# Kernel tuning notes

Hardware: AMD Instinct MI355X
Metric: run time of the kernel (lower is better)

The kernel has to match this reference:

```python
import jax, jax.numpy as jnp
import numpy as np

L, B, N_IN, N_OUT, BIDIR, K = 2048, 16, 256, 256, 2, 6


def setup_inputs() -> dict:
    key = jax.random.key(0)
    k1, k2 = jax.random.split(key, 2)
    x = jax.random.normal(k1, (L, B, N_IN), jnp.float32)
    val = (6.0 / (N_IN + N_OUT)) ** 0.5
    weight_in = jax.random.uniform(k2, (N_IN, BIDIR * N_OUT * K), jnp.float32, -val, val)
    bias_in = jnp.zeros((K * BIDIR * N_OUT,), jnp.float32)
    c1_init = jnp.zeros((B, BIDIR * N_OUT), jnp.float32)
    c2_init = jnp.zeros((B, BIDIR * N_OUT), jnp.float32)
    d_init = jnp.zeros((B, BIDIR * N_OUT), jnp.float32)
    return {"x": x, "weight_in": weight_in, "bias_in": bias_in,
            "c1_init": c1_init, "c2_init": c2_init, "d_init": d_init}


def _flip_dir1(a):
    # reverse time for the backward direction (dir index 1)
    return a.at[:, :, 1].set(jnp.flip(a[:, :, 1], axis=0))


def _sopa_forward(x, weight_in, bias_in, c1_init, c2_init, d_init):
    length, batch = x.shape[0], x.shape[1]
    # u_: [L, B, bidir, n_out, k]
    u = (x.reshape(-1, N_IN) @ weight_in).reshape(length, batch, BIDIR, N_OUT, K)
    bias = bias_in.reshape(K, BIDIR, N_OUT)  # [k, bidir, n_out]
    x1, x2, x3 = u[..., 0], u[..., 1], u[..., 2]
    f1 = jax.nn.sigmoid(u[..., 3] + bias[3])
    f2 = jax.nn.sigmoid(u[..., 4] + bias[4])
    # selfloop gate sigmoid(u[...,5]+bias[5]) is computed in the original but
    # unused by the recurrence, so it is omitted here (no effect on outputs).

    # flip time for direction 1 so one scan handles both directions
    x1f, x2f, x3f, f1f, f2f = (_flip_dir1(a) for a in (x1, x2, x3, f1, f2))

    c1_0 = c1_init.reshape(batch, BIDIR, N_OUT)
    c2_0 = c2_init.reshape(batch, BIDIR, N_OUT)
    d_0 = d_init.reshape(batch, BIDIR, N_OUT)

    def step(carry, inp):
        c1, c2, d = carry
        x1t, x2t, x3t, f1t, f2t = inp
        c1n = (c1 - x1t) * f1t + x1t
        tmp = x3t * d
        c2n = (c2 - tmp) * f2t + tmp
        return (c1n, c2n, x2t), (c1n, c2n)

    (c1_f, c2_f, d_f), (c1s, c2s) = jax.lax.scan(
        step, (c1_0, c2_0, d_0), (x1f, x2f, x3f, f1f, f2f))

    c1s = _flip_dir1(c1s)
    c2s = _flip_dir1(c2s)
    return (c1s, c2s,
            c1_f.reshape(batch, -1), c2_f.reshape(batch, -1), d_f.reshape(batch, -1))


def reference(x, weight_in, bias_in, c1_init, c2_init, d_init):
    return _sopa_forward(x, weight_in, bias_in, c1_init, c2_init, d_init)
```

## Files before the change

### kernel.cpp

```cpp
#include <hip/hip_runtime.h>
#include <cstdint>
#include <cstddef>

typedef unsigned short u16;
typedef unsigned int u32;
typedef __bf16 bf16x8 __attribute__((ext_vector_type(8)));
typedef float f32x4 __attribute__((ext_vector_type(4)));

#define SL 2048
#define NCH 8192
#define SEGS 64

#define OFF_C2S 16777216
#define OFF_C1F 33554432
#define OFF_C2F 33562624
#define OFF_DF  33570816

__device__ __forceinline__ u16 f2bf(float f) {
  union { float f; u32 i; } v; v.f = f;
  u32 x = v.i;
  return (u16)((x + 0x7fffu + ((x >> 16) & 1u)) >> 16);
}
__device__ __forceinline__ u32 cvtpk(float lo, float hi) {
  u32 r;
  asm("v_cvt_pk_bf16_f32 %0, %1, %2" : "=v"(r) : "v"(lo), "v"(hi));
  return r;
}
__device__ __forceinline__ float sigmoidf(float v) {
  return 1.f / (1.f + __expf(-v));
}

__global__ __launch_bounds__(256) void xconv_kernel(
    const float* __restrict__ x, u16* __restrict__ xb) {
  int t8 = blockIdx.x * 256 + threadIdx.x;
  int b  = t8 & 15;
  int kb = (t8 >> 4) & 31;
  int ot = t8 >> 9;
  const float* src = x + (((size_t)(ot * 16 + b)) << 8) + kb * 8;
  f32x4 a = *(const f32x4*)src;
  f32x4 c = *(const f32x4*)(src + 4);
  union { bf16x8 v; u32 u[4]; } h;
  h.u[0] = cvtpk(a[0], a[1]);
  h.u[1] = cvtpk(a[2], a[3]);
  h.u[2] = cvtpk(c[0], c[1]);
  h.u[3] = cvtpk(c[2], c[3]);
  *(bf16x8*)(xb + ((size_t)ot << 12) + kb * 128 + b * 8) = h.v;
}

__global__ __launch_bounds__(256) void repack_kernel(
    const float* __restrict__ W, u16* __restrict__ Wt) {
  int idx = blockIdx.x * 256 + threadIdx.x;
  int col = idx % 3072;
  int kk  = idx / 3072;
  float w = W[idx];
  int d    = (col >= 1536) ? 1 : 0;
  int col2 = col - d * 1536;
  int n = col2 / 6;
  int p = col2 - n * 6;
  if (p >= 5) return;
  int ch2 = d * 256 + n;
  int cg = ch2 >> 4, l15 = ch2 & 15;
  int kk8 = kk & 7, q = kk >> 3;
  int l4 = q & 3, h = (q >> 2) & 1, kt = q >> 3;
  size_t dst = ((size_t)(p * 256 + cg * 8 + kt * 2 + h)) * 512 +
               (l4 * 16 + l15) * 8 + kk8;
  Wt[dst] = f2bf(w);
}

__global__ __launch_bounds__(256, 2) void fusedA_kernel(
    const u16* __restrict__ xb, const u16* __restrict__ Wt,
    const float* __restrict__ bias,
    float* __restrict__ A1, float* __restrict__ B1,
    float* __restrict__ A2, float* __restrict__ B2k,
    float* __restrict__ G2, float* __restrict__ X2B) {
  const int tid = threadIdx.x;
  const int lane = tid & 63;
  const int wc = tid >> 6;
  const int l15 = lane & 15, l4 = lane >> 4;
  const int bid = blockIdx.x;
  const int xcd = bid & 7;
  const int j = bid >> 3;
  const int s = xcd * 8 + (j & 7);
  const int bc = j >> 3;
  const int dir = bc >> 2;
  const int ch2 = bc * 64 + wc * 16 + l15;
  const int fb0 = (bc * 4 + wc) * 8;

  const float bv3 = bias[1536 + ch2];
  const float bv4 = bias[2048 + ch2];

  float a1[4], b1[4], a2[4], b2[4], g2[4], x2p[4];
#pragma unroll
  for (int r = 0; r < 4; ++r) {
    a1[r] = 1.f; b1[r] = 0.f; a2[r] = 1.f; b2[r] = 0.f;
    g2[r] = 0.f; x2p[r] = 0.f;
  }

  for (int rt = 0; rt < 8; ++rt) {
    const u16* ab0; const u16* ab1; const u16* ab2; const u16* ab3;
    {
      int tf = s * 32 + rt * 4;
      int o0 = dir ? (SL - 1 - tf) : tf;
      int o1 = dir ? (o0 - 1) : (o0 + 1);
      int o2 = dir ? (o0 - 2) : (o0 + 2);
      int o3 = dir ? (o0 - 3) : (o0 + 3);
      size_t lo = (size_t)(l4 * 128 + l15 * 8);
      ab0 = xb + ((size_t)o0 << 12) + lo;
      ab1 = xb + ((size_t)o1 << 12) + lo;
      ab2 = xb + ((size_t)o2 << 12) + lo;
      ab3 = xb + ((size_t)o3 << 12) + lo;
    }

    f32x4 acc[5][4];
#pragma unroll
    for (int p = 0; p < 5; ++p)
#pragma unroll
      for (int i = 0; i < 4; ++i) acc[p][i] = (f32x4){0.f, 0.f, 0.f, 0.f};

#pragma unroll
    for (int kt = 0; kt < 4; ++kt) {
#pragma unroll
      for (int h = 0; h < 2; ++h) {
        const int kb4 = (kt * 8 + h * 4) * 128;
        bf16x8 af[4];
        af[0] = *(const bf16x8*)(ab0 + kb4);
        af[1] = *(const bf16x8*)(ab1 + kb4);
        af[2] = *(const bf16x8*)(ab2 + kb4);
        af[3] = *(const bf16x8*)(ab3 + kb4);
        const int fb = fb0 + kt * 2 + h;
#pragma unroll
        for (int p = 0; p < 5; ++p) {
          bf16x8 bfr = *(const bf16x8*)(
              Wt + (size_t)(p * 256 + fb) * 512 + lane * 8);
#pragma unroll
          for (int i = 0; i < 4; ++i)
            acc[p][i] = __builtin_amdgcn_mfma_f32_16x16x32_bf16(
                af[i], bfr, acc[p][i], 0, 0, 0);
        }
      }
    }

    const bool first = (rt == 0);
#pragma unroll
    for (int i = 0; i < 4; ++i) {
#pragma unroll
      for (int r = 0; r < 4; ++r) {
        float x1 = acc[0][i][r], x2v = acc[1][i][r], x3 = acc[2][i][r];
        float f1 = sigmoidf(acc[3][i][r] + bv3);
        float f2 = sigmoidf(acc[4][i][r] + bv4);
        a1[r] *= f1;
        b1[r] = f1 * b1[r] + (1.f - f1) * x1;
        float tmp = x3 * x2p[r];
        a2[r] *= f2;
        b2[r] = f2 * b2[r] + (1.f - f2) * tmp;
        g2[r] = (first && i == 0) ? (1.f - f2) * x3 : g2[r] * f2;
        x2p[r] = x2v;
      }
    }
  }

  const size_t oo = (size_t)s * NCH + (size_t)ch2 * 16 + l4 * 4;
  *(f32x4*)(A1  + oo) = (f32x4){a1[0], a1[1], a1[2], a1[3]};
  *(f32x4*)(B1  + oo) = (f32x4){b1[0], b1[1], b1[2], b1[3]};
  *(f32x4*)(A2  + oo) = (f32x4){a2[0], a2[1], a2[2], a2[3]};
  *(f32x4*)(B2k + oo) = (f32x4){b2[0], b2[1], b2[2], b2[3]};
  *(f32x4*)(G2  + oo) = (f32x4){g2[0], g2[1], g2[2], g2[3]};
  *(f32x4*)(X2B + oo) = (f32x4){x2p[0], x2p[1], x2p[2], x2p[3]};
}

__global__ __launch_bounds__(256) void scanB_kernel(
    const float* __restrict__ A1, const float* __restrict__ B1,
    const float* __restrict__ A2, const float* __restrict__ B2k,
    const float* __restrict__ G2, const float* __restrict__ X2B,
    const float* __restrict__ c1_init, const float* __restrict__ c2_init,
    const float* __restrict__ d_init,
    float* __restrict__ C1c, float* __restrict__ C2c,
    float* __restrict__ out) {
  int t = blockIdx.x * 256 + threadIdx.x;
  int ch2 = t >> 4, b = t & 15;
  int ch = b * 512 + ch2;
  float c1 = c1_init[ch], c2 = c2_init[ch], d0 = d_init[ch];
#pragma unroll 8
  for (int s = 0; s < SEGS; ++s) {
    int o = s * NCH + t;
    C1c[o] = c1; C2c[o] = c2;
    c1 = A1[o] * c1 + B1[o];
    c2 = A2[o] * c2 + (B2k[o] + G2[o] * d0);
    d0 = X2B[o];
  }
  out[OFF_C1F + ch] = c1;
  out[OFF_C2F + ch] = c2;
  out[OFF_DF + ch] = d0;
}

__global__ __launch_bounds__(256, 2) void fusedC_kernel(
    const u16* __restrict__ xb, const u16* __restrict__ Wt,
    const float* __restrict__ bias, const float* __restrict__ d_init,
    const float* __restrict__ X2B,
    const float* __restrict__ C1c, const float* __restrict__ C2c,
    float* __restrict__ out) {
  const int tid = threadIdx.x;
  const int lane = tid & 63;
  const int wc = tid >> 6;
  const int l15 = lane & 15, l4 = lane >> 4;
  const int bid = blockIdx.x;
  const int xcd = bid & 7;
  const int j = bid >> 3;
  const int s = xcd * 8 + (j & 7);
  const int bc = j >> 3;
  const int dir = bc >> 2;
  const int ch2 = bc * 64 + wc * 16 + l15;
  const int fb0 = (bc * 4 + wc) * 8;

  const float bv3 = bias[1536 + ch2];
  const float bv4 = bias[2048 + ch2];

  const int chb = (l4 * 4) * 512 + ch2;
  float c1[4], c2[4], x2p[4];
  {
    const size_t oo = (size_t)s * NCH + (size_t)ch2 * 16 + l4 * 4;
    f32x4 u0 = *(const f32x4*)(C1c + oo);
    f32x4 w0 = *(const f32x4*)(C2c + oo);
#pragma unroll
    for (int r = 0; r < 4; ++r) { c1[r] = u0[r]; c2[r] = w0[r]; }
    if (s == 0) {
#pragma unroll
      for (int r = 0; r < 4; ++r) x2p[r] = d_init[chb + r * 512];
    } else {
      f32x4 xv = *(const f32x4*)(X2B + oo - NCH);
#pragma unroll
      for (int r = 0; r < 4; ++r) x2p[r] = xv[r];
    }
  }

  for (int rt = 0; rt < 8; ++rt) {
    const u16* ab0; const u16* ab1; const u16* ab2; const u16* ab3;
    {
      int tf = s * 32 + rt * 4;
      int o0 = dir ? (SL - 1 - tf) : tf;
      int o1 = dir ? (o0 - 1) : (o0 + 1);
      int o2 = dir ? (o0 - 2) : (o0 + 2);
      int o3 = dir ? (o0 - 3) : (o0 + 3);
      size_t lo = (size_t)(l4 * 128 + l15 * 8);
      ab0 = xb + ((size_t)o0 << 12) + lo;
      ab1 = xb + ((size_t)o1 << 12) + lo;
      ab2 = xb + ((size_t)o2 << 12) + lo;
      ab3 = xb + ((size_t)o3 << 12) + lo;
    }

    f32x4 acc[5][4];
#pragma unroll
    for (int p = 0; p < 5; ++p)
#pragma unroll
      for (int i = 0; i < 4; ++i) acc[p][i] = (f32x4){0.f, 0.f, 0.f, 0.f};

#pragma unroll
    for (int kt = 0; kt < 4; ++kt) {
#pragma unroll
      for (int h = 0; h < 2; ++h) {
        const int kb4 = (kt * 8 + h * 4) * 128;
        bf16x8 af[4];
        af[0] = *(const bf16x8*)(ab0 + kb4);
        af[1] = *(const bf16x8*)(ab1 + kb4);
        af[2] = *(const bf16x8*)(ab2 + kb4);
        af[3] = *(const bf16x8*)(ab3 + kb4);
        const int fb = fb0 + kt * 2 + h;
#pragma unroll
        for (int p = 0; p < 5; ++p) {
          bf16x8 bfr = *(const bf16x8*)(
              Wt + (size_t)(p * 256 + fb) * 512 + lane * 8);
#pragma unroll
          for (int i = 0; i < 4; ++i)
            acc[p][i] = __builtin_amdgcn_mfma_f32_16x16x32_bf16(
                af[i], bfr, acc[p][i], 0, 0, 0);
        }
      }
    }

#pragma unroll
    for (int i = 0; i < 4; ++i) {
      int tfl = s * 32 + rt * 4 + i;
      int t_out = dir ? (SL - 1 - tfl) : tfl;
      float* orow = out + (size_t)t_out * NCH + chb;
#pragma unroll
      for (int r = 0; r < 4; ++r) {
        float x1 = acc[0][i][r], x2v = acc[1][i][r], x3 = acc[2][i][r];
        float f1 = sigmoidf(acc[3][i][r] + bv3);
        float f2 = sigmoidf(acc[4][i][r] + bv4);
        c1[r] = f1 * c1[r] + (1.f - f1) * x1;
        float tmp = x3 * x2p[r];
        c2[r] = f2 * c2[r] + (1.f - f2) * tmp;
        x2p[r] = x2v;
        __builtin_nontemporal_store(c1[r], orow + r * 512);
        __builtin_nontemporal_store(c2[r], orow + OFF_C2S + (size_t)r * 512);
      }
    }
  }
}

extern "C" void kernel_launch(void* const* d_in, const int* in_sizes, int n_in,
                              void* d_out, int out_size, void* d_ws, size_t ws_size,
                              hipStream_t stream) {
  const float* x    = (const float*)d_in[0];
  const float* W    = (const float*)d_in[1];
  const float* bias = (const float*)d_in[2];
  const float* c1i  = (const float*)d_in[3];
  const float* c2i  = (const float*)d_in[4];
  const float* di   = (const float*)d_in[5];
  float* out = (float*)d_out;

  uint8_t* w8 = (uint8_t*)d_ws;
  u16* Wt  = (u16*)w8;
  u16* xb  = (u16*)(w8 + 1310720ull);
  float* X2B = (float*)(w8 + 18087936ull);
  float* A1  = (float*)(w8 + 20185088ull);
  float* B1  = A1  + SEGS * NCH;
  float* A2  = B1  + SEGS * NCH;
  float* B2k = A2  + SEGS * NCH;
  float* G2  = B2k + SEGS * NCH;
  float* C1c = G2  + SEGS * NCH;
  float* C2c = C1c + SEGS * NCH;

  hipLaunchKernelGGL(xconv_kernel, dim3(4096), dim3(256), 0, stream, x, xb);
  hipLaunchKernelGGL(repack_kernel, dim3(3072), dim3(256), 0, stream, W, Wt);
  hipLaunchKernelGGL(fusedA_kernel, dim3(512), dim3(256), 0, stream,
                     xb, Wt, bias, A1, B1, A2, B2k, G2, X2B);
  hipLaunchKernelGGL(scanB_kernel, dim3(32), dim3(256), 0, stream,
                     A1, B1, A2, B2k, G2, X2B, c1i, c2i, di, C1c, C2c, out);
  hipLaunchKernelGGL(fusedC_kernel, dim3(512), dim3(256), 0, stream,
                     xb, Wt, bias, di, X2B, C1c, C2c, out);
}
```

Baseline: 363.3 us.

## Split c1 and c2 recurrences into separate blocks and precompute segment-end x2

Adds a small kernel that computes x2 at the last step of each segment. This lets the c2 segment scan start from the true previous d value instead of carrying a separate G2 correction term. The fused A and C kernels now use twice as many blocks: one half handles the c1 path (two projections), the other the c2 path (three projections). The split lowers registers per block and allows higher occupancy (launch bounds 4). In exchange, each x row is loaded by both halves and there is an extra launch.

```diff
diff --git a/kernel.cpp b/kernel.cpp
--- a/kernel.cpp
+++ b/kernel.cpp
@@ -67,133 +67,185 @@
   Wt[dst] = f2bf(w);
 }
 
-__global__ __launch_bounds__(256, 2) void fusedA_kernel(
+__global__ __launch_bounds__(256) void x2seg_kernel(
     const u16* __restrict__ xb, const u16* __restrict__ Wt,
-    const float* __restrict__ bias,
+    float* __restrict__ X2B) {
+  const int tid = threadIdx.x;
+  const int lane = tid & 63;
+  const int wc = tid >> 6;
+  const int l15 = lane & 15, l4 = lane >> 4;
+  const int s = blockIdx.x;
+  const int bc = blockIdx.y;
+  const int dir = bc >> 2;
+  const int ch2 = bc * 64 + wc * 16 + l15;
+  const int fb0 = (bc * 4 + wc) * 8;
+  int tf = s * 32 + 31;
+  int ot = dir ? (SL - 1 - tf) : tf;
+  const u16* ab = xb + ((size_t)ot << 12) + l4 * 128 + l15 * 8;
+  f32x4 acc = (f32x4){0.f, 0.f, 0.f, 0.f};
+#pragma unroll
+  for (int kt = 0; kt < 4; ++kt)
+#pragma unroll
+    for (int h = 0; h < 2; ++h) {
+      const int kb4 = (kt * 8 + h * 4) * 128;
+      bf16x8 af = *(const bf16x8*)(ab + kb4);
+      bf16x8 bfr = *(const bf16x8*)(
+          Wt + (size_t)(1 * 256 + fb0 + kt * 2 + h) * 512 + lane * 8);
+      acc = __builtin_amdgcn_mfma_f32_16x16x32_bf16(af, bfr, acc, 0, 0, 0);
+    }
+  *(f32x4*)(X2B + (size_t)s * NCH + (size_t)ch2 * 16 + l4 * 4) = acc;
+}
+
+__global__ __launch_bounds__(256, 4) void fusedA_kernel(
+    const u16* __restrict__ xb, const u16* __restrict__ Wt,
+    const float* __restrict__ bias, const float* __restrict__ d_init,
+    const float* __restrict__ X2B,
     float* __restrict__ A1, float* __restrict__ B1,
-    float* __restrict__ A2, float* __restrict__ B2k,
-    float* __restrict__ G2, float* __restrict__ X2B) {
+    float* __restrict__ A2, float* __restrict__ B2) {
   const int tid = threadIdx.x;
   const int lane = tid & 63;
   const int wc = tid >> 6;
   const int l15 = lane & 15, l4 = lane >> 4;
   const int bid = blockIdx.x;
   const int xcd = bid & 7;
-  const int j = bid >> 3;
+  const int r2 = bid >> 3;
+  const int part = r2 & 1;
+  const int j = r2 >> 1;
   const int s = xcd * 8 + (j & 7);
   const int bc = j >> 3;
   const int dir = bc >> 2;
   const int ch2 = bc * 64 + wc * 16 + l15;
   const int fb0 = (bc * 4 + wc) * 8;
-
-  const float bv3 = bias[1536 + ch2];
-  const float bv4 = bias[2048 + ch2];
-
-  float a1[4], b1[4], a2[4], b2[4], g2[4], x2p[4];
-#pragma unroll
-  for (int r = 0; r < 4; ++r) {
-    a1[r] = 1.f; b1[r] = 0.f; a2[r] = 1.f; b2[r] = 0.f;
-    g2[r] = 0.f; x2p[r] = 0.f;
-  }
-
-  for (int rt = 0; rt < 8; ++rt) {
-    const u16* ab0; const u16* ab1; const u16* ab2; const u16* ab3;
-    {
+  const size_t lo = (size_t)(l4 * 128 + l15 * 8);
+  const size_t oo = (size_t)s * NCH + (size_t)ch2 * 16 + l4 * 4;
+
+  if (part == 0) {
+    const float bv3 = bias[1536 + ch2];
+    float a1[4] = {1.f, 1.f, 1.f, 1.f}, b1[4] = {0.f, 0.f, 0.f, 0.f};
+    for (int rt = 0; rt < 8; ++rt) {
       int tf = s * 32 + rt * 4;
       int o0 = dir ? (SL - 1 - tf) : tf;
-      int o1 = dir ? (o0 - 1) : (o0 + 1);
-      int o2 = dir ? (o0 - 2) : (o0 + 2);
-      int o3 = dir ? (o0 - 3) : (o0 + 3);
-      size_t lo = (size_t)(l4 * 128 + l15 * 8);
-      ab0 = xb + ((size_t)o0 << 12) + lo;
-      ab1 = xb + ((size_t)o1 << 12) + lo;
-      ab2 = xb + ((size_t)o2 << 12) + lo;
-      ab3 = xb + ((size_t)o3 << 12) + lo;
-    }
-
-    f32x4 acc[5][4];
-#pragma unroll
-    for (int p = 0; p < 5; ++p)
-#pragma unroll
-      for (int i = 0; i < 4; ++i) acc[p][i] = (f32x4){0.f, 0.f, 0.f, 0.f};
-
-#pragma unroll
-    for (int kt = 0; kt < 4; ++kt) {
-#pragma unroll
-      for (int h = 0; h < 2; ++h) {
-        const int kb4 = (kt * 8 + h * 4) * 128;
-        bf16x8 af[4];
-        af[0] = *(const bf16x8*)(ab0 + kb4);
-        af[1] = *(const bf16x8*)(ab1 + kb4);
-        af[2] = *(const bf16x8*)(ab2 + kb4);
-        af[3] = *(const bf16x8*)(ab3 + kb4);
-        const int fb = fb0 + kt * 2 + h;
-#pragma unroll
-        for (int p = 0; p < 5; ++p) {
-          bf16x8 bfr = *(const bf16x8*)(
-              Wt + (size_t)(p * 256 + fb) * 512 + lane * 8);
-#pragma unroll
-          for (int i = 0; i < 4; ++i)
-            acc[p][i] = __builtin_amdgcn_mfma_f32_16x16x32_bf16(
-                af[i], bfr, acc[p][i], 0, 0, 0);
-        }
-      }
-    }
-
-    const bool first = (rt == 0);
-#pragma unroll
-    for (int i = 0; i < 4; ++i) {
-#pragma unroll
-      for (int r = 0; r < 4; ++r) {
-        float x1 = acc[0][i][r], x2v = acc[1][i][r], x3 = acc[2][i][r];
-        float f1 = sigmoidf(acc[3][i][r] + bv3);
-        float f2 = sigmoidf(acc[4][i][r] + bv4);
-        a1[r] *= f1;
-        b1[r] = f1 * b1[r] + (1.f - f1) * x1;
-        float tmp = x3 * x2p[r];
-        a2[r] *= f2;
-        b2[r] = f2 * b2[r] + (1.f - f2) * tmp;
-        g2[r] = (first && i == 0) ? (1.f - f2) * x3 : g2[r] * f2;
-        x2p[r] = x2v;
-      }
-    }
+      int st = dir ? -1 : 1;
+      const u16* ab[4];
+#pragma unroll
+      for (int i = 0; i < 4; ++i)
+        ab[i] = xb + ((size_t)(o0 + i * st) << 12) + lo;
+      f32x4 acc0[4], acc3[4];
+#pragma unroll
+      for (int i = 0; i < 4; ++i) {
+        acc0[i] = (f32x4){0.f, 0.f, 0.f, 0.f};
+        acc3[i] = (f32x4){0.f, 0.f, 0.f, 0.f};
+      }
+#pragma unroll
+      for (int kt = 0; kt < 4; ++kt)
+#pragma unroll
+        for (int h = 0; h < 2; ++h) {
+          const int kb4 = (kt * 8 + h * 4) * 128;
+          const int fb = fb0 + kt * 2 + h;
+          bf16x8 w0 = *(const bf16x8*)(Wt + (size_t)(fb) * 512 + lane * 8);
+          bf16x8 w3 = *(const bf16x8*)(Wt + (size_t)(768 + fb) * 512 + lane * 8);
+#pragma unroll
+          for (int i = 0; i < 4; ++i) {
+            bf16x8 af = *(const bf16x8*)(ab[i] + kb4);
+            acc0[i] = __builtin_amdgcn_mfma_f32_16x16x32_bf16(af, w0, acc0[i], 0, 0, 0);
+            acc3[i] = __builtin_amdgcn_mfma_f32_16x16x32_bf16(af, w3, acc3[i], 0, 0, 0);
+          }
+        }
+#pragma unroll
+      for (int i = 0; i < 4; ++i)
+#pragma unroll
+        for (int r = 0; r < 4; ++r) {
+          float f1 = sigmoidf(acc3[i][r] + bv3);
+          a1[r] *= f1;
+          b1[r] = f1 * b1[r] + (1.f - f1) * acc0[i][r];
+        }
+    }
+    *(f32x4*)(A1 + oo) = (f32x4){a1[0], a1[1], a1[2], a1[3]};
+    *(f32x4*)(B1 + oo) = (f32x4){b1[0], b1[1], b1[2], b1[3]};
+  } else {
+    const float bv4 = bias[2048 + ch2];
+    const int chb = (l4 * 4) * 512 + ch2;
+    float a2[4] = {1.f, 1.f, 1.f, 1.f}, b2[4] = {0.f, 0.f, 0.f, 0.f}, x2p[4];
+    if (s == 0) {
+#pragma unroll
+      for (int r = 0; r < 4; ++r) x2p[r] = d_init[chb + r * 512];
+    } else {
+      f32x4 xv = *(const f32x4*)(X2B + oo - NCH);
+#pragma unroll
+      for (int r = 0; r < 4; ++r) x2p[r] = xv[r];
+    }
+    for (int rt = 0; rt < 8; ++rt) {
+      int tf = s * 32 + rt * 4;
+      int o0 = dir ? (SL - 1 - tf) : tf;
+      int st = dir ? -1 : 1;
+      const u16* ab[4];
+#pragma unroll
+      for (int i = 0; i < 4; ++i)
+        ab[i] = xb + ((size_t)(o0 + i * st) << 12) + lo;
+      f32x4 acc1[4], acc2[4], acc4[4];
+#pragma unroll
+      for (int i = 0; i < 4; ++i) {
+        acc1[i] = (f32x4){0.f, 0.f, 0.f, 0.f};
+        acc2[i] = (f32x4){0.f, 0.f, 0.f, 0.f};
+        acc4[i] = (f32x4){0.f, 0.f, 0.f, 0.f};
+      }
+#pragma unroll
+      for (int kt = 0; kt < 4; ++kt)
+#pragma unroll
+        for (int h = 0; h < 2; ++h) {
+          const int kb4 = (kt * 8 + h * 4) * 128;
+          const int fb = fb0 + kt * 2 + h;
+          bf16x8 w1 = *(const bf16x8*)(Wt + (size_t)(256 + fb) * 512 + lane * 8);
+          bf16x8 w2 = *(const bf16x8*)(Wt + (size_t)(512 + fb) * 512 + lane * 8);
+          bf16x8 w4 = *(const bf16x8*)(Wt + (size_t)(1024 + fb) * 512 + lane * 8);
+#pragma unroll
+          for (int i = 0; i < 4; ++i) {
+            bf16x8 af = *(const bf16x8*)(ab[i] + kb4);
+            acc1[i] = __builtin_amdgcn_mfma_f32_16x16x32_bf16(af, w1, acc1[i], 0, 0, 0);
+            acc2[i] = __builtin_amdgcn_mfma_f32_16x16x32_bf16(af, w2, acc2[i], 0, 0, 0);
+            acc4[i] = __builtin_amdgcn_mfma_f32_16x16x32_bf16(af, w4, acc4[i], 0, 0, 0);
+          }
+        }
+#pragma unroll
+      for (int i = 0; i < 4; ++i)
+#pragma unroll
+        for (int r = 0; r < 4; ++r) {
+          float f2 = sigmoidf(acc4[i][r] + bv4);
+          float tmp = acc2[i][r] * x2p[r];
+          a2[r] *= f2;
+          b2[r] = f2 * b2[r] + (1.f - f2) * tmp;
+          x2p[r] = acc1[i][r];
+        }
+    }
+    *(f32x4*)(A2 + oo) = (f32x4){a2[0], a2[1], a2[2], a2[3]};
+    *(f32x4*)(B2 + oo) = (f32x4){b2[0], b2[1], b2[2], b2[3]};
   }
-
-  const size_t oo = (size_t)s * NCH + (size_t)ch2 * 16 + l4 * 4;
-  *(f32x4*)(A1  + oo) = (f32x4){a1[0], a1[1], a1[2], a1[3]};
-  *(f32x4*)(B1  + oo) = (f32x4){b1[0], b1[1], b1[2], b1[3]};
-  *(f32x4*)(A2  + oo) = (f32x4){a2[0], a2[1], a2[2], a2[3]};
-  *(f32x4*)(B2k + oo) = (f32x4){b2[0], b2[1], b2[2], b2[3]};
-  *(f32x4*)(G2  + oo) = (f32x4){g2[0], g2[1], g2[2], g2[3]};
-  *(f32x4*)(X2B + oo) = (f32x4){x2p[0], x2p[1], x2p[2], x2p[3]};
 }
 
 __global__ __launch_bounds__(256) void scanB_kernel(
     const float* __restrict__ A1, const float* __restrict__ B1,
-    const float* __restrict__ A2, const float* __restrict__ B2k,
-    const float* __restrict__ G2, const float* __restrict__ X2B,
+    const float* __restrict__ A2, const float* __restrict__ B2,
+    const float* __restrict__ X2B,
     const float* __restrict__ c1_init, const float* __restrict__ c2_init,
-    const float* __restrict__ d_init,
     float* __restrict__ C1c, float* __restrict__ C2c,
     float* __restrict__ out) {
   int t = blockIdx.x * 256 + threadIdx.x;
   int ch2 = t >> 4, b = t & 15;
   int ch = b * 512 + ch2;
-  float c1 = c1_init[ch], c2 = c2_init[ch], d0 = d_init[ch];
+  float c1 = c1_init[ch], c2 = c2_init[ch];
 #pragma unroll 8
   for (int s = 0; s < SEGS; ++s) {
     int o = s * NCH + t;
     C1c[o] = c1; C2c[o] = c2;
     c1 = A1[o] * c1 + B1[o];
-    c2 = A2[o] * c2 + (B2k[o] + G2[o] * d0);
-    d0 = X2B[o];
+    c2 = A2[o] * c2 + B2[o];
   }
   out[OFF_C1F + ch] = c1;
   out[OFF_C2F + ch] = c2;
-  out[OFF_DF + ch] = d0;
-}
-
-__global__ __launch_bounds__(256, 2) void fusedC_kernel(
+  out[OFF_DF + ch] = X2B[(size_t)63 * NCH + t];
+}
+
+__global__ __launch_bounds__(256, 4) void fusedC_kernel(
     const u16* __restrict__ xb, const u16* __restrict__ Wt,
     const float* __restrict__ bias, const float* __restrict__ d_init,
     const float* __restrict__ X2B,
@@ -205,94 +257,129 @@
   const int l15 = lane & 15, l4 = lane >> 4;
   const int bid = blockIdx.x;
   const int xcd = bid & 7;
-  const int j = bid >> 3;
+  const int r2 = bid >> 3;
+  const int part = r2 & 1;
+  const int j = r2 >> 1;
   const int s = xcd * 8 + (j & 7);
   const int bc = j >> 3;
   const int dir = bc >> 2;
   const int ch2 = bc * 64 + wc * 16 + l15;
   const int fb0 = (bc * 4 + wc) * 8;
-
-  const float bv3 = bias[1536 + ch2];
-  const float bv4 = bias[2048 + ch2];
-
+  const size_t lo = (size_t)(l4 * 128 + l15 * 8);
+  const size_t oo = (size_t)s * NCH + (size_t)ch2 * 16 + l4 * 4;
   const int chb = (l4 * 4) * 512 + ch2;
-  float c1[4], c2[4], x2p[4];
-  {
-    const size_t oo = (size_t)s * NCH + (size_t)ch2 * 16 + l4 * 4;
-    f32x4 u0 = *(const f32x4*)(C1c + oo);
-    f32x4 w0 = *(const f32x4*)(C2c + oo);
-#pragma unroll
-    for (int r = 0; r < 4; ++r) { c1[r] = u0[r]; c2[r] = w0[r]; }
-    if (s == 0) {
-#pragma unroll
-      for (int r = 0; r < 4; ++r) x2p[r] = d_init[chb + r * 512];
-    } else {
-      f32x4 xv = *(const f32x4*)(X2B + oo - NCH);
-#pragma unroll
-      for (int r = 0; r < 4; ++r) x2p[r] = xv[r];
-    }
-  }
-
-  for (int rt = 0; rt < 8; ++rt) {
-    const u16* ab0; const u16* ab1; const u16* ab2; const u16* ab3;
+
+  if (part == 0) {
+    const float bv3 = bias[1536 + ch2];
+    float c1[4];
     {
+      f32x4 u0 = *(const f32x4*)(C1c + oo);
+#pragma unroll
+      for (int r = 0; r < 4; ++r) c1[r] = u0[r];
+    }
+    for (int rt = 0; rt < 8; ++rt) {
       int tf = s * 32 + rt * 4;
       int o0 = dir ? (SL - 1 - tf) : tf;
-      int o1 = dir ? (o0 - 1) : (o0 + 1);
-      int o2 = dir ? (o0 - 2) : (o0 + 2);
-      int o3 = dir ? (o0 - 3) : (o0 + 3);
-      size_t lo = (size_t)(l4 * 128 + l15 * 8);
-      ab0 = xb + ((size_t)o0 << 12) + lo;
-      ab1 = xb + ((size_t)o1 << 12) + lo;
-      ab2 = xb + ((size_t)o2 << 12) + lo;
-      ab3 = xb + ((size_t)o3 << 12) + lo;
-    }
-
-    f32x4 acc[5][4];
-#pragma unroll
-    for (int p = 0; p < 5; ++p)
-#pragma unroll
-      for (int i = 0; i < 4; ++i) acc[p][i] = (f32x4){0.f, 0.f, 0.f, 0.f};
-
-#pragma unroll
-    for (int kt = 0; kt < 4; ++kt) {
-#pragma unroll
-      for (int h = 0; h < 2; ++h) {
-        const int kb4 = (kt * 8 + h * 4) * 128;
-        bf16x8 af[4];
-        af[0] = *(const bf16x8*)(ab0 + kb4);
-        af[1] = *(const bf16x8*)(ab1 + kb4);
-        af[2] = *(const bf16x8*)(ab2 + kb4);
-        af[3] = *(const bf16x8*)(ab3 + kb4);
-        const int fb = fb0 + kt * 2 + h;
-#pragma unroll
-        for (int p = 0; p < 5; ++p) {
-          bf16x8 bfr = *(const bf16x8*)(
-              Wt + (size_t)(p * 256 + fb) * 512 + lane * 8);
-#pragma unroll
-          for (int i = 0; i < 4; ++i)
-            acc[p][i] = __builtin_amdgcn_mfma_f32_16x16x32_bf16(
-                af[i], bfr, acc[p][i], 0, 0, 0);
-        }
-      }
-    }
-
-#pragma unroll
-    for (int i = 0; i < 4; ++i) {
-      int tfl = s * 32 + rt * 4 + i;
-      int t_out = dir ? (SL - 1 - tfl) : tfl;
-      float* orow = out + (size_t)t_out * NCH + chb;
-#pragma unroll
-      for (int r = 0; r < 4; ++r) {
-        float x1 = acc[0][i][r], x2v = acc[1][i][r], x3 = acc[2][i][r];
-        float f1 = sigmoidf(acc[3][i][r] + bv3);
-        float f2 = sigmoidf(acc[4][i][r] + bv4);
-        c1[r] = f1 * c1[r] + (1.f - f1) * x1;
-        float tmp = x3 * x2p[r];
-        c2[r] = f2 * c2[r] + (1.f - f2) * tmp;
-        x2p[r] = x2v;
-        __builtin_nontemporal_store(c1[r], orow + r * 512);
-        __builtin_nontemporal_store(c2[r], orow + OFF_C2S + (size_t)r * 512);
+      int st = dir ? -1 : 1;
+      const u16* ab[4];
+#pragma unroll
+      for (int i = 0; i < 4; ++i)
+        ab[i] = xb + ((size_t)(o0 + i * st) << 12) + lo;
+      f32x4 acc0[4], acc3[4];
+#pragma unroll
+      for (int i = 0; i < 4; ++i) {
+        acc0[i] = (f32x4){0.f, 0.f, 0.f, 0.f};
+        acc3[i] = (f32x4){0.f, 0.f, 0.f, 0.f};
+      }
+#pragma unroll
+      for (int kt = 0; kt < 4; ++kt)
+#pragma unroll
+        for (int h = 0; h < 2; ++h) {
+          const int kb4 = (kt * 8 + h * 4) * 128;
+          const int fb = fb0 + kt * 2 + h;
+          bf16x8 w0 = *(const bf16x8*)(Wt + (size_t)(fb) * 512 + lane * 8);
+          bf16x8 w3 = *(const bf16x8*)(Wt + (size_t)(768 + fb) * 512 + lane * 8);
+#pragma unroll
+          for (int i = 0; i < 4; ++i) {
+            bf16x8 af = *(const bf16x8*)(ab[i] + kb4);
+            acc0[i] = __builtin_amdgcn_mfma_f32_16x16x32_bf16(af, w0, acc0[i], 0, 0, 0);
+            acc3[i] = __builtin_amdgcn_mfma_f32_16x16x32_bf16(af, w3, acc3[i], 0, 0, 0);
+          }
+        }
+#pragma unroll
+      for (int i = 0; i < 4; ++i) {
+        int tfl = s * 32 + rt * 4 + i;
+        int t_out = dir ? (SL - 1 - tfl) : tfl;
+        float* orow = out + (size_t)t_out * NCH + chb;
+#pragma unroll
+        for (int r = 0; r < 4; ++r) {
+          float f1 = sigmoidf(acc3[i][r] + bv3);
+          c1[r] = f1 * c1[r] + (1.f - f1) * acc0[i][r];
+          __builtin_nontemporal_store(c1[r], orow + (size_t)r * 512);
+        }
+      }
+    }
+  } else {
+    const float bv4 = bias[2048 + ch2];
+    float c2[4], x2p[4];
+    {
+      f32x4 w0 = *(const f32x4*)(C2c + oo);
+#pragma unroll
+      for (int r = 0; r < 4; ++r) c2[r] = w0[r];
+      if (s == 0) {
+#pragma unroll
+        for (int r = 0; r < 4; ++r) x2p[r] = d_init[chb + r * 512];
+      } else {
+        f32x4 xv = *(const f32x4*)(X2B + oo - NCH);
+#pragma unroll
+        for (int r = 0; r < 4; ++r) x2p[r] = xv[r];
+      }
+    }
+    for (int rt = 0; rt < 8; ++rt) {
+      int tf = s * 32 + rt * 4;
+      int o0 = dir ? (SL - 1 - tf) : tf;
+      int st = dir ? -1 : 1;
+      const u16* ab[4];
+#pragma unroll
+      for (int i = 0; i < 4; ++i)
+        ab[i] = xb + ((size_t)(o0 + i * st) << 12) + lo;
+      f32x4 acc1[4], acc2[4], acc4[4];
+#pragma unroll
+      for (int i = 0; i < 4; ++i) {
+        acc1[i] = (f32x4){0.f, 0.f, 0.f, 0.f};
+        acc2[i] = (f32x4){0.f, 0.f, 0.f, 0.f};
+        acc4[i] = (f32x4){0.f, 0.f, 0.f, 0.f};
+      }
+#pragma unroll
+      for (int kt = 0; kt < 4; ++kt)
+#pragma unroll
+        for (int h = 0; h < 2; ++h) {
+          const int kb4 = (kt * 8 + h * 4) * 128;
+          const int fb = fb0 + kt * 2 + h;
+          bf16x8 w1 = *(const bf16x8*)(Wt + (size_t)(256 + fb) * 512 + lane * 8);
+          bf16x8 w2 = *(const bf16x8*)(Wt + (size_t)(512 + fb) * 512 + lane * 8);
+          bf16x8 w4 = *(const bf16x8*)(Wt + (size_t)(1024 + fb) * 512 + lane * 8);
+#pragma unroll
+          for (int i = 0; i < 4; ++i) {
+            bf16x8 af = *(const bf16x8*)(ab[i] + kb4);
+            acc1[i] = __builtin_amdgcn_mfma_f32_16x16x32_bf16(af, w1, acc1[i], 0, 0, 0);
+            acc2[i] = __builtin_amdgcn_mfma_f32_16x16x32_bf16(af, w2, acc2[i], 0, 0, 0);
+            acc4[i] = __builtin_amdgcn_mfma_f32_16x16x32_bf16(af, w4, acc4[i], 0, 0, 0);
+          }
+        }
+#pragma unroll
+      for (int i = 0; i < 4; ++i) {
+        int tfl = s * 32 + rt * 4 + i;
+        int t_out = dir ? (SL - 1 - tfl) : tfl;
+        float* orow = out + (size_t)t_out * NCH + chb + OFF_C2S;
+#pragma unroll
+        for (int r = 0; r < 4; ++r) {
+          float f2 = sigmoidf(acc4[i][r] + bv4);
+          float tmp = acc2[i][r] * x2p[r];
+          c2[r] = f2 * c2[r] + (1.f - f2) * tmp;
+          x2p[r] = acc1[i][r];
+          __builtin_nontemporal_store(c2[r], orow + (size_t)r * 512);
+        }
       }
     }
   }
@@ -316,17 +403,18 @@
   float* A1  = (float*)(w8 + 20185088ull);
   float* B1  = A1  + SEGS * NCH;
   float* A2  = B1  + SEGS * NCH;
-  float* B2k = A2  + SEGS * NCH;
-  float* G2  = B2k + SEGS * NCH;
-  float* C1c = G2  + SEGS * NCH;
+  float* B2  = A2  + SEGS * NCH;
+  float* C1c = B2  + SEGS * NCH;
   float* C2c = C1c + SEGS * NCH;
 
   hipLaunchKernelGGL(xconv_kernel, dim3(4096), dim3(256), 0, stream, x, xb);
   hipLaunchKernelGGL(repack_kernel, dim3(3072), dim3(256), 0, stream, W, Wt);
-  hipLaunchKernelGGL(fusedA_kernel, dim3(512), dim3(256), 0, stream,
-                     xb, Wt, bias, A1, B1, A2, B2k, G2, X2B);
+  hipLaunchKernelGGL(x2seg_kernel, dim3(64, 8), dim3(256), 0, stream,
+                     xb, Wt, X2B);
+  hipLaunchKernelGGL(fusedA_kernel, dim3(1024), dim3(256), 0, stream,
+                     xb, Wt, bias, di, X2B, A1, B1, A2, B2);
   hipLaunchKernelGGL(scanB_kernel, dim3(32), dim3(256), 0, stream,
-                     A1, B1, A2, B2k, G2, X2B, c1i, c2i, di, C1c, C2c, out);
-  hipLaunchKernelGGL(fusedC_kernel, dim3(512), dim3(256), 0, stream,
+                     A1, B1, A2, B2, X2B, c1i, c2i, C1c, C2c, out);
+  hipLaunchKernelGGL(fusedC_kernel, dim3(1024), dim3(256), 0, stream,
                      xb, Wt, bias, di, X2B, C1c, C2c, out);
 }
```

Result: slower. 410.5 us (+13.0%).
